# Kernel optimization log

Measured on AMD Instinct MI355X. Metric: run time of the kernel, lower is better.

The kernel has to match this reference:

```python
import jax, jax.numpy as jnp
import numpy as np

N_ENTITY = 100000
N_RELATION = 64
DIM = 16
N_HOP = 2
N_MEM = 32
N_NODES = 16384


def setup_inputs() -> dict:
    key = jax.random.key(0)
    ks = jax.random.split(key, 7)
    return {
        "nodes": jax.random.randint(ks[0], (N_NODES,), 0, N_ENTITY),
        "memories_h": jax.random.randint(ks[1], (N_HOP, N_NODES, N_MEM), 0, N_ENTITY),
        "memories_r": jax.random.randint(ks[2], (N_HOP, N_NODES, N_MEM), 0, N_RELATION),
        "memories_t": jax.random.randint(ks[3], (N_HOP, N_NODES, N_MEM), 0, N_ENTITY),
        "entity_emb": jax.random.normal(ks[4], (N_ENTITY, DIM), jnp.float32) * 0.1,
        "relation_emb": jax.random.normal(ks[5], (N_RELATION, DIM * DIM), jnp.float32) * 0.1,
        "W": jax.random.normal(ks[6], (DIM, DIM), jnp.float32) * 0.1,
    }


def reference(nodes, memories_h, memories_r, memories_t, entity_emb, relation_emb, W):
    # item embeddings for the query nodes: [N, D]
    item = entity_emb[nodes]
    o_list = []
    for hop in range(N_HOP):  # small fixed hop count (2)
        h = entity_emb[memories_h[hop]]                                  # [N, M, D]
        r = relation_emb[memories_r[hop]].reshape(-1, N_MEM, DIM, DIM)   # [N, M, D, D]
        t = entity_emb[memories_t[hop]]                                  # [N, M, D]
        # Rh = R @ h : [N, M, D]
        Rh = jnp.einsum('nmde,nme->nmd', r, h)
        # attention over the n_memory slots (softmax dim=0 per node in original)
        probs = jax.nn.softmax(jnp.einsum('nmd,nd->nm', Rh, item), axis=1)
        # weighted sum of tails: [N, D]
        o = jnp.einsum('nm,nmd->nd', probs, t)
        # item_update_mode == 'plus_transform': Linear(dim, dim, bias=False)
        item = (item + o) @ W.T
        o_list.append(o)
    # Faithful to the original torch in-place semantics: at hop 0 the line
    # `kg_feature += o_list[0]` doubles o0 in place; the final result for
    # n_hop=2 is therefore o1 + 2*o0.
    return o_list[1] + 2.0 * o_list[0]
```

## Files before the change

### kernel.cpp

```cpp
#include <hip/hip_runtime.h>

#define NE     100000
#define NR     64
#define DIM    16
#define NHOP   2
#define NMEM   32
#define NNODES 16384

#define WPITCH 20

static __device__ __forceinline__ float bflo(unsigned u) {
    union { unsigned i; float f; } c; c.i = u << 16; return c.f;
}
static __device__ __forceinline__ float bfhi(unsigned u) {
    union { unsigned i; float f; } c; c.i = u & 0xffff0000u; return c.f;
}
static __device__ __forceinline__ unsigned short f2bf(float f) {
    union { float f; unsigned u; } c; c.f = f;
    unsigned u = c.u;
    return (unsigned short)((u + 0x7fffu + ((u >> 16) & 1u)) >> 16);
}

static __device__ __forceinline__ float dpp_sum16(float v) {
    union { int i; float f; } a, b;
    a.f = v;
    b.i = __builtin_amdgcn_update_dpp(0, a.i, 0xB1,  0xf, 0xf, true); a.f += b.f;
    b.i = __builtin_amdgcn_update_dpp(0, a.i, 0x4E,  0xf, 0xf, true); a.f += b.f;
    b.i = __builtin_amdgcn_update_dpp(0, a.i, 0x124, 0xf, 0xf, true); a.f += b.f;
    b.i = __builtin_amdgcn_update_dpp(0, a.i, 0x128, 0xf, 0xf, true); a.f += b.f;
    return a.f;
}

static __device__ __forceinline__ float bcast(float v, int l) {
    return __int_as_float(__builtin_amdgcn_readlane(__float_as_int(v), l));
}

extern "C" __global__ void __launch_bounds__(512, 8)
ripple_kernel(const int* __restrict__ nodes,
              const int* __restrict__ mh,
              const int* __restrict__ mr,
              const int* __restrict__ mt,
              const float* __restrict__ ent,
              const float* __restrict__ rel,
              const float* __restrict__ W,
              float* __restrict__ out)
{
    __shared__ __align__(16) unsigned short rt[NR * 256];
    __shared__ __align__(16) float ws[DIM * WPITCH];

    const int tid = threadIdx.x;

    {
        const float4* rel4 = (const float4*)rel;
        #pragma unroll
        for (int i = 0; i < 8; ++i) {
            int vidx = i * 512 + tid;
            float4 v = rel4[vidx];
            int k0 = vidx * 4;
            int r  = k0 >> 8;
            int k  = k0 & 255;
            int d  = k >> 4;
            int e0 = k & 15;
            int phys = ((d >> 2) + (e0 >> 2)) & 3;
            unsigned short* p = &rt[r * 256 + e0 * 16 + phys * 4 + (d & 3)];
            p[0]  = f2bf(v.x);
            p[16] = f2bf(v.y);
            p[32] = f2bf(v.z);
            p[48] = f2bf(v.w);
        }
        if (tid < 256) ws[(tid >> 4) * WPITCH + (tid & 15)] = W[tid];
    }
    __syncthreads();

    const int lane = tid & 63;
    const int wid  = tid >> 6;
    const int g    = lane >> 4;
    const int e    = lane & 15;
    const int n    = blockIdx.x * 8 + wid;

    int voff[4];
    {
        const int s = e >> 2;
        #pragma unroll
        for (int j = 0; j < 4; ++j)
            voff[j] = e * 32 + (((j + s) & 3) << 3);
    }

    float item    = ent[nodes[n] * DIM + e];
    float out_acc = 0.f;

    #pragma unroll
    for (int hop = 0; hop < NHOP; ++hop) {
        float itm[16];
        #pragma unroll
        for (int d = 0; d < 16; ++d) itm[d] = bcast(item, d);

        const int ibase = hop * (NNODES * NMEM) + n * NMEM;
        float sc[8], tv[8];

        #pragma unroll
        for (int it = 0; it < 8; ++it) {
            const int m    = it * 4 + g;
            const int hidx = mh[ibase + m];
            const int ridx = mr[ibase + m];
            const int tidx = mt[ibase + m];

            const char* rbase = (const char*)rt + (ridx << 9);
            float q = 0.f;
            #pragma unroll
            for (int j = 0; j < 4; ++j) {
                uint2 u = *(const uint2*)(rbase + voff[j]);
                q += itm[4 * j + 0] * bflo(u.x) + itm[4 * j + 1] * bfhi(u.x)
                   + itm[4 * j + 2] * bflo(u.y) + itm[4 * j + 3] * bfhi(u.y);
            }
            float he = ent[hidx * DIM + e];
            sc[it] = dpp_sum16(q * he);
            tv[it] = ent[tidx * DIM + e];
        }

        float Z = 0.f;
        #pragma unroll
        for (int it = 0; it < 8; ++it) { sc[it] = __expf(sc[it]); Z += sc[it]; }
        Z += __shfl_xor(Z, 16);
        Z += __shfl_xor(Z, 32);
        const float inv = 1.f / Z;

        float o = 0.f;
        #pragma unroll
        for (int it = 0; it < 8; ++it) o += sc[it] * tv[it];
        o *= inv;
        o += __shfl_xor(o, 16);
        o += __shfl_xor(o, 32);

        out_acc += (hop == 0) ? 2.f * o : o;

        const float v = item + o;
        float nit = 0.f;
        const float4* wr = (const float4*)&ws[e * WPITCH];
        #pragma unroll
        for (int j = 0; j < 4; ++j) {
            float4 w = wr[j];
            nit += w.x * bcast(v, 4 * j + 0) + w.y * bcast(v, 4 * j + 1)
                 + w.z * bcast(v, 4 * j + 2) + w.w * bcast(v, 4 * j + 3);
        }
        item = nit;
    }

    if (lane < 16) out[n * DIM + e] = out_acc;
}

extern "C" void kernel_launch(void* const* d_in, const int* in_sizes, int n_in,
                              void* d_out, int out_size, void* d_ws, size_t ws_size,
                              hipStream_t stream) {
    const int*   nodes = (const int*)d_in[0];
    const int*   mh    = (const int*)d_in[1];
    const int*   mr    = (const int*)d_in[2];
    const int*   mt    = (const int*)d_in[3];
    const float* ent   = (const float*)d_in[4];
    const float* rel   = (const float*)d_in[5];
    const float* W     = (const float*)d_in[6];
    float*       out   = (float*)d_out;

    dim3 grid(NNODES / 8);
    dim3 block(512);
    ripple_kernel<<<grid, block, 0, stream>>>(nodes, mh, mr, mt, ent, rel, W, out);
}
```

Baseline: 102.0 us.

## Use fp16 relation table with fdot2 and vectorize memory index loads

Stores the relation matrices in LDS as fp16 instead of bf16 and computes the R·item dot product with packed fp16 dot2 instructions, using item values packed into half2 registers. Memory slots are reassigned so each 16-lane group handles 8 contiguous slots, which lets h/r/t indices be fetched with int4 vector loads. All entity gathers are issued before the compute loop to overlap latency. The cost is reduced precision of item in fp16 and higher register pressure from the prefetched values.

```diff
diff --git a/kernel.cpp b/kernel.cpp
--- a/kernel.cpp
+++ b/kernel.cpp
@@ -9,16 +9,19 @@
 
 #define WPITCH 20
 
-static __device__ __forceinline__ float bflo(unsigned u) {
-    union { unsigned i; float f; } c; c.i = u << 16; return c.f;
+typedef __attribute__((ext_vector_type(2))) _Float16 half2_t;
+
+static __device__ __forceinline__ half2_t as_h2(unsigned u) {
+    union { unsigned i; half2_t h; } c; c.i = u; return c.h;
 }
-static __device__ __forceinline__ float bfhi(unsigned u) {
-    union { unsigned i; float f; } c; c.i = u & 0xffff0000u; return c.f;
-}
-static __device__ __forceinline__ unsigned short f2bf(float f) {
-    union { float f; unsigned u; } c; c.f = f;
-    unsigned u = c.u;
-    return (unsigned short)((u + 0x7fffu + ((u >> 16) & 1u)) >> 16);
+
+static __device__ __forceinline__ float qdot2(unsigned u, unsigned ip, float q) {
+#if __has_builtin(__builtin_amdgcn_fdot2)
+    return __builtin_amdgcn_fdot2(as_h2(u), as_h2(ip), q, false);
+#else
+    half2_t a = as_h2(u), b = as_h2(ip);
+    return q + (float)a.x * (float)b.x + (float)a.y * (float)b.y;
+#endif
 }
 
 static __device__ __forceinline__ float dpp_sum16(float v) {
@@ -33,6 +36,16 @@
 
 static __device__ __forceinline__ float bcast(float v, int l) {
     return __int_as_float(__builtin_amdgcn_readlane(__float_as_int(v), l));
+}
+
+static __device__ __forceinline__ unsigned short f2h(float f) {
+    union { _Float16 h; unsigned short s; } c; c.h = (_Float16)f; return c.s;
+}
+
+static __device__ __forceinline__ unsigned pack2h(float a, float b) {
+    union { _Float16 h[2]; unsigned u; } c;
+    c.h[0] = (_Float16)a; c.h[1] = (_Float16)b;
+    return c.u;
 }
 
 extern "C" __global__ void __launch_bounds__(512, 8)
@@ -63,10 +76,10 @@
             int e0 = k & 15;
             int phys = ((d >> 2) + (e0 >> 2)) & 3;
             unsigned short* p = &rt[r * 256 + e0 * 16 + phys * 4 + (d & 3)];
-            p[0]  = f2bf(v.x);
-            p[16] = f2bf(v.y);
-            p[32] = f2bf(v.z);
-            p[48] = f2bf(v.w);
+            p[0]  = f2h(v.x);
+            p[16] = f2h(v.y);
+            p[32] = f2h(v.z);
+            p[48] = f2h(v.w);
         }
         if (tid < 256) ws[(tid >> 4) * WPITCH + (tid & 15)] = W[tid];
     }
@@ -91,31 +104,39 @@
 
     #pragma unroll
     for (int hop = 0; hop < NHOP; ++hop) {
-        float itm[16];
+        unsigned ip[8];
         #pragma unroll
-        for (int d = 0; d < 16; ++d) itm[d] = bcast(item, d);
+        for (int j = 0; j < 8; ++j)
+            ip[j] = pack2h(bcast(item, 2 * j), bcast(item, 2 * j + 1));
 
-        const int ibase = hop * (NNODES * NMEM) + n * NMEM;
-        float sc[8], tv[8];
+        const int ibase = hop * (NNODES * NMEM) + n * NMEM + g * 8;
+        int hi[8], ri[8], ti[8];
+        {
+            const int4* p;
+            p = (const int4*)(mh + ibase); ((int4*)hi)[0] = p[0]; ((int4*)hi)[1] = p[1];
+            p = (const int4*)(mr + ibase); ((int4*)ri)[0] = p[0]; ((int4*)ri)[1] = p[1];
+            p = (const int4*)(mt + ibase); ((int4*)ti)[0] = p[0]; ((int4*)ti)[1] = p[1];
+        }
 
+        float hv[8], tv[8];
         #pragma unroll
         for (int it = 0; it < 8; ++it) {
-            const int m    = it * 4 + g;
-            const int hidx = mh[ibase + m];
-            const int ridx = mr[ibase + m];
-            const int tidx = mt[ibase + m];
+            hv[it] = ent[hi[it] * DIM + e];
+            tv[it] = ent[ti[it] * DIM + e];
+        }
 
-            const char* rbase = (const char*)rt + (ridx << 9);
+        float sc[8];
+        #pragma unroll
+        for (int it = 0; it < 8; ++it) {
+            const char* rbase = (const char*)rt + (ri[it] << 9);
             float q = 0.f;
             #pragma unroll
             for (int j = 0; j < 4; ++j) {
                 uint2 u = *(const uint2*)(rbase + voff[j]);
-                q += itm[4 * j + 0] * bflo(u.x) + itm[4 * j + 1] * bfhi(u.x)
-                   + itm[4 * j + 2] * bflo(u.y) + itm[4 * j + 3] * bfhi(u.y);
+                q = qdot2(u.x, ip[2 * j + 0], q);
+                q = qdot2(u.y, ip[2 * j + 1], q);
             }
-            float he = ent[hidx * DIM + e];
-            sc[it] = dpp_sum16(q * he);
-            tv[it] = ent[tidx * DIM + e];
+            sc[it] = dpp_sum16(q * hv[it]);
         }
 
         float Z = 0.f;
```

Measured after the change: 103.5 us. About the same (+1.5%).
